# Performance work log

Hardware: AMD Instinct MI355X
Metric: run time of the kernel (lower is better)

## Reference

```python
import jax, jax.numpy as jnp
import numpy as np

BS, S, D, N, E = 16, 8, 10, 32, 300
H, STATE_DIM, MID, OC = 128, 96, 256, 100

def setup_inputs():
    ks = jax.random.split(jax.random.key(0), 24)
    g = lambda i, shape: (0.02 * jax.random.normal(ks[i], shape)).astype(jnp.float32)
    return {
        "stock_news": jax.random.normal(ks[0], (BS, S, D, N, E), dtype=jnp.float32),
        "stock_feats": jax.random.normal(ks[1], (BS, STATE_DIM), dtype=jnp.float32),
        "conv_w3": g(2, (S, OC, E, 3)), "conv_b3": g(3, (S, OC)),
        "conv_w4": g(4, (S, OC, E, 4)), "conv_b4": g(5, (S, OC)),
        "conv_w5": g(6, (S, OC, E, 5)), "conv_b5": g(7, (S, OC)),
        "w_ih": g(8, (S, 4 * H, 3 * OC)), "w_hh": g(9, (S, 4 * H, H)),
        "b_ih": g(10, (S, 4 * H)), "b_hh": g(11, (S, 4 * H)),
        "linX_w": g(12, (S, H, 2 * H)), "linX_b": g(13, (S, H)),
        "linY_w": g(14, (S, 64, H)), "linY_b": g(15, (S, 64)),
        "w1": g(16, (24, STATE_DIM)), "b1": g(17, (24,)),
        "w2": g(18, (16, 24)), "b2": g(19, (16,)),
        "arch_w1": g(20, (MID, 16 + 64 * S)), "arch_b1": g(21, (MID,)),
        "arch_w2": g(22, (S, MID)), "arch_b2": g(23, (S,)),
        "action_var": jnp.full((S,), -0.25, dtype=jnp.float32),
    }

def _conv_maxpool(x, w, b, k):
    # x: [S,B,D,N,E], w: [S,OC,E,k] -> conv1d over news axis then max-pool -> [S,B,D,OC]
    L = x.shape[3] - k + 1
    y = jnp.broadcast_to(b[:, None, None, None, :], (x.shape[0], x.shape[1], x.shape[2], L, w.shape[1]))
    for j in range(k):
        y = y + jnp.einsum('sbdne,soe->sbdno', x[:, :, :, j:j + L, :], w[:, :, :, j])
    return y.max(axis=3)

def _lstm_attn(xs, w_ih, w_hh, b_ih, b_hh):
    # single-stock LSTM (batch_first) + attention from original code; xs: [B,D,I] -> [B,2H]
    pre = jnp.einsum('bdi,gi->dbg', xs, w_ih) + b_ih + b_hh  # [D,B,4H]
    h0 = jnp.zeros((xs.shape[0], w_hh.shape[1]), xs.dtype)
    def step(carry, g_t):
        h, c = carry
        gates = g_t + h @ w_hh.T
        i, f, g, o = jnp.split(gates, 4, axis=-1)  # PyTorch gate order i,f,g,o
        c = jax.nn.sigmoid(f) * c + jax.nn.sigmoid(i) * jnp.tanh(g)
        h = jax.nn.sigmoid(o) * jnp.tanh(c)
        return (h, c), h
    (hn, _), outs = jax.lax.scan(step, (h0, h0), pre)
    outs = outs.transpose(1, 0, 2)  # [B,D,H]
    w = jnp.einsum('bh,bdh->bd', hn, outs)[:, None, :]  # [B,1,D]
    w = jax.nn.softmax(w, axis=1)  # softmax over singleton dim, exactly as torch code (yields ones)
    out = jnp.sum(w.transpose(0, 2, 1) * outs, axis=1)  # [B,H]
    return jnp.concatenate([hn, out], axis=-1)  # [B,2H]

def _forward(stock_news, stock_feats, conv_w3, conv_b3, conv_w4, conv_b4, conv_w5, conv_b5,
             w_ih, w_hh, b_ih, b_hh, linX_w, linX_b, linY_w, linY_b,
             w1, b1, w2, b2, arch_w1, arch_b1, arch_w2, arch_b2, action_var):
    x = stock_news.transpose(1, 0, 2, 3, 4)  # [S,B,D,N,E]
    feats = [_conv_maxpool(x, w, b, k) for (w, b, k) in
             ((conv_w3, conv_b3, 3), (conv_w4, conv_b4, 4), (conv_w5, conv_b5, 5))]
    text = jnp.concatenate(feats, axis=-1)  # [S,B,D,300]
    comb = jax.vmap(_lstm_attn)(text, w_ih, w_hh, b_ih, b_hh)  # [S,B,2H]
    hX = jax.nn.relu(jnp.einsum('sbi,shi->sbh', comb, linX_w) + linX_b[:, None, :])  # dropout is eval-mode identity
    hY = jax.nn.relu(jnp.einsum('sbh,soh->sbo', hX, linY_w) + linY_b[:, None, :])  # [S,B,64]
    stock_text = hY.transpose(1, 0, 2).reshape(stock_news.shape[0], -1)  # [B,S*64]
    f = jax.nn.relu(stock_feats @ w1.T + b1) @ w2.T + b2  # [B,16]
    total = jnp.concatenate([stock_text, f], axis=-1)  # [B,16+64S]
    mu = jnp.tanh(jax.nn.relu(total @ arch_w1.T + arch_b1) @ arch_w2.T + arch_b2)
    return mu, jnp.exp(action_var)

def reference(stock_news, stock_feats, conv_w3, conv_b3, conv_w4, conv_b4, conv_w5, conv_b5,
              w_ih, w_hh, b_ih, b_hh, linX_w, linX_b, linY_w, linY_b,
              w1, b1, w2, b2, arch_w1, arch_b1, arch_w2, arch_b2, action_var):
    return _forward(stock_news, stock_feats, conv_w3, conv_b3, conv_w4, conv_b4, conv_w5, conv_b5,
                    w_ih, w_hh, b_ih, b_hh, linX_w, linX_b, linY_w, linY_b,
                    w1, b1, w2, b2, arch_w1, arch_b1, arch_w2, arch_b2, action_var)
```

## Files before the change

kernel.cpp:

```cpp
#include <hip/hip_runtime.h>
#include <math.h>

#define S_   8
#define B_   16
#define D_   10
#define N_   32
#define E_   300
#define H_   128
#define G4_  512
#define SDIM_ 96
#define MID_ 256
#define TOT_ 528

#define NWPACK 3850240
#define NWPRE  1310720

typedef unsigned short u16;
typedef __attribute__((ext_vector_type(8))) short short8;
typedef __attribute__((ext_vector_type(4))) short short4v;
typedef __attribute__((ext_vector_type(4))) float f32x4;

static __device__ __forceinline__ u16 f2bf(float f) {
    unsigned u = __builtin_bit_cast(unsigned, f);
    return (u16)((u + 0x7FFFu + ((u >> 16) & 1u)) >> 16);
}

__global__ void prep(const float* __restrict__ w3, const float* __restrict__ b3,
                     const float* __restrict__ w4, const float* __restrict__ b4,
                     const float* __restrict__ w5, const float* __restrict__ b5,
                     const float* __restrict__ w_ih,
                     const float* __restrict__ lxw, const float* __restrict__ lyw,
                     const float* __restrict__ aw1,
                     u16* __restrict__ wpack2, u16* __restrict__ wpre2,
                     float* __restrict__ bcomb,
                     float* __restrict__ lxwT, float* __restrict__ lywT,
                     float* __restrict__ aw1T) {
    int idx = blockIdx.x * blockDim.x + threadIdx.x;
    if (idx < NWPACK) {
        int j = idx & 7, q = (idx >> 3) & 3;
        int rest = idx >> 5;
        int c = rest % 320, ks = (rest / 320) % 47, s = rest / 15040;
        int kk = ks * 32 + q * 8 + j;
        int tap = kk / 300, e = kk - tap * 300;
        float v = 0.f;
        if (tap < 5) {
            if (c < 100)      { if (tap < 3) v = w3[((s*100 + c      )*300 + e)*3 + tap]; }
            else if (c < 200) { if (tap < 4) v = w4[((s*100 + c - 100)*300 + e)*4 + tap]; }
            else if (c < 300) {              v = w5[((s*100 + c - 200)*300 + e)*5 + tap]; }
        }
        wpack2[idx] = f2bf(v);
    } else if (idx < NWPACK + NWPRE) {
        int i2 = idx - NWPACK;
        int j = i2 & 7, q = (i2 >> 3) & 3;
        int rest = i2 >> 5;
        int g = rest & 511, ks = (rest >> 9) % 10, s = rest / 5120;
        int kk = ks * 32 + q * 8 + j;
        float v = (kk < 300) ? w_ih[((size_t)s * 512 + g) * 300 + kk] : 0.f;
        wpre2[i2] = f2bf(v);
    }
    if (idx < 262144) {
        int t = idx & 127, i = (idx >> 7) & 255, s = idx >> 15;
        lxwT[idx] = lxw[((size_t)(s * 128 + t)) * 256 + i];
    }
    if (idx < 65536) {
        int t = idx & 63, i = (idx >> 6) & 127, s = idx >> 13;
        lywT[idx] = lyw[((size_t)(s * 64 + t)) * 128 + i];
    }
    if (idx < 135168) {
        int j = idx & 255, i = idx >> 8;
        aw1T[idx] = aw1[(size_t)j * TOT_ + i];
    }
    if (idx < 2560) {
        int c = idx % 320, s = idx / 320;
        float bv = 0.f;
        if (c < 100)      bv = b3[s*100 + c];
        else if (c < 200) bv = b4[s*100 + c - 100];
        else if (c < 300) bv = b5[s*100 + c - 200];
        bcomb[idx] = bv;
    }
}

__global__ __launch_bounds__(256, 2) void conv_mfma(const float* __restrict__ news,
                                                    const u16* __restrict__ wpack2,
                                                    const float* __restrict__ bcomb,
                                                    u16* __restrict__ text_bf) {
    __shared__ u16 xs[2 * 10816];
    const int tid = threadIdx.x, bid = blockIdx.x;
    const int s = bid & 7, b2d = bid >> 3, b2 = b2d / 10, d = b2d % 10;
    const int l = tid & 63, w = tid >> 6, q = l >> 4, r16 = l & 15;

    const u16* gp[5];
#pragma unroll
    for (int nt = 0; nt < 5; ++nt) {
        int c = w * 80 + nt * 16 + r16;
        gp[nt] = wpack2 + (size_t)s * 481280 + c * 32 + q * 8;
    }

    short8 bf0[5], bf1[5];
#pragma unroll
    for (int nt = 0; nt < 5; ++nt) bf0[nt] = *reinterpret_cast<const short8*>(gp[nt]);
#pragma unroll
    for (int nt = 0; nt < 5; ++nt) bf1[nt] = *reinterpret_cast<const short8*>(gp[nt] + 10240);

#pragma unroll
    for (int sm = 0; sm < 2; ++sm) {
        const float4* xg = reinterpret_cast<const float4*>(
            news + (size_t)(((b2 * 2 + sm) * 8 + s) * 10 + d) * 9600);
        for (int i = tid; i < 2704; i += 256) {
            ushort4 u;
            if (i < 2400) {
                float4 v = xg[i];
                u.x = f2bf(v.x); u.y = f2bf(v.y); u.z = f2bf(v.z); u.w = f2bf(v.w);
            } else { u.x = 0; u.y = 0; u.z = 0; u.w = 0; }
            *reinterpret_cast<ushort4*>(&xs[sm * 10816 + 4 * i]) = u;
        }
    }
    __syncthreads();

    f32x4 acc[4][5];
#pragma unroll
    for (int m = 0; m < 4; ++m)
#pragma unroll
        for (int nt = 0; nt < 5; ++nt) acc[m][nt] = (f32x4)(0.f);

#define LOADA(dst, ks) do {                                                     \
    _Pragma("unroll")                                                           \
    for (int m_ = 0; m_ < 4; ++m_) {                                            \
        int off_ = (m_ >> 1) * 10816 + ((m_ & 1) * 16 + r16) * 300 + (ks) * 32 + q * 8; \
        short4v lo_ = *reinterpret_cast<const short4v*>(&xs[off_]);             \
        short4v hi_ = *reinterpret_cast<const short4v*>(&xs[off_ + 4]);         \
        dst[m_] = __builtin_shufflevector(lo_, hi_, 0, 1, 2, 3, 4, 5, 6, 7);    \
    } } while (0)

#define MFMAS(bfv, av) do {                                                     \
    __builtin_amdgcn_s_setprio(1);                                              \
    _Pragma("unroll")                                                           \
    for (int m_ = 0; m_ < 4; ++m_)                                              \
        _Pragma("unroll")                                                       \
        for (int nt_ = 0; nt_ < 5; ++nt_)                                       \
            acc[m_][nt_] = __builtin_amdgcn_mfma_f32_16x16x32_bf16(av[m_], bfv[nt_], acc[m_][nt_], 0, 0, 0); \
    __builtin_amdgcn_s_setprio(0);                                              \
    } while (0)

    short8 a0[4], a1[4];
    LOADA(a0, 0);
    for (int ks = 0; ks < 46; ks += 2) {
        LOADA(a1, ks + 1);
        MFMAS(bf0, a0);
#pragma unroll
        for (int nt = 0; nt < 5; ++nt)
            bf0[nt] = *reinterpret_cast<const short8*>(gp[nt] + (ks + 2) * 10240);

        LOADA(a0, ks + 2);
        MFMAS(bf1, a1);
        if (ks + 3 < 47) {
#pragma unroll
            for (int nt = 0; nt < 5; ++nt)
                bf1[nt] = *reinterpret_cast<const short8*>(gp[nt] + (ks + 3) * 10240);
        }
    }
    MFMAS(bf0, a0);
#undef LOADA
#undef MFMAS

#pragma unroll
    for (int sm = 0; sm < 2; ++sm) {
        const size_t trow = ((size_t)(s * 16 + b2 * 2 + sm) * 10 + d) * 320;
#pragma unroll
        for (int nt = 0; nt < 5; ++nt) {
            int oc = w * 80 + nt * 16 + r16;
            int L = (oc < 100) ? 30 : (oc < 200) ? 29 : 28;
            float mx = -3e38f;
#pragma unroll
            for (int r = 0; r < 4; ++r) {
                mx = fmaxf(mx, acc[sm * 2][nt][r]);
                int row1 = 16 + q * 4 + r;
                if (row1 < L) mx = fmaxf(mx, acc[sm * 2 + 1][nt][r]);
            }
            mx = fmaxf(mx, __shfl_xor(mx, 16));
            mx = fmaxf(mx, __shfl_xor(mx, 32));
            if (l < 16)
                text_bf[trow + oc] = f2bf(mx + bcomb[s * 320 + oc]);
        }
    }
}

__global__ __launch_bounds__(256) void lstm_pre_mfma(const u16* __restrict__ text_bf,
                                                     const u16* __restrict__ wpre2,
                                                     const float* __restrict__ b_ih,
                                                     const float* __restrict__ b_hh,
                                                     float* __restrict__ pre) {
    __shared__ u16 as16[16 * 320];
    const int sd = blockIdx.x, s = sd / 10, d = sd % 10;
    const int tid = threadIdx.x, l = tid & 63, w = tid >> 6, q = l >> 4, r16 = l & 15;

    for (int i = tid; i < 640; i += 256) {
        int r = i / 40, c = i % 40;
        *reinterpret_cast<float4*>(as16 + r * 320 + ((c ^ (r & 7)) << 3)) =
            *reinterpret_cast<const float4*>(text_bf + ((size_t)(s * 16 + r) * 10 + d) * 320 + c * 8);
    }
    __syncthreads();

    const u16* gpb[8];
#pragma unroll
    for (int nt = 0; nt < 8; ++nt) {
        int g = w * 128 + nt * 16 + r16;
        gpb[nt] = wpre2 + (size_t)s * 163840 + g * 32 + q * 8;
    }

    f32x4 acc[8];
#pragma unroll
    for (int nt = 0; nt < 8; ++nt) acc[nt] = (f32x4)(0.f);

    for (int ks = 0; ks < 10; ++ks) {
        short8 a = *reinterpret_cast<const short8*>(
            as16 + r16 * 320 + (((ks * 4 + q) ^ (r16 & 7)) << 3));
#pragma unroll
        for (int nt = 0; nt < 8; ++nt) {
            short8 bf = *reinterpret_cast<const short8*>(gpb[nt] + ks * 16384);
            acc[nt] = __builtin_amdgcn_mfma_f32_16x16x32_bf16(a, bf, acc[nt], 0, 0, 0);
        }
    }

#pragma unroll
    for (int nt = 0; nt < 8; ++nt) {
        int g = w * 128 + nt * 16 + r16;
        float bias = b_ih[s * 512 + g] + b_hh[s * 512 + g];
#pragma unroll
        for (int r = 0; r < 4; ++r) {
            int brow = q * 4 + r;
            pre[((size_t)sd * 16 + brow) * 512 + g] = acc[nt][r] + bias;
        }
    }
}

__global__ __launch_bounds__(512) void lstm_tail(const float* __restrict__ pre,
                                                 const float* __restrict__ w_hh,
                                                 const float* __restrict__ lxwT, const float* __restrict__ lxb,
                                                 const float* __restrict__ lywT, const float* __restrict__ lyb,
                                                 float* __restrict__ total) {
    __shared__ float wchunk[128][129];
    __shared__ float h_lds[H_];
    __shared__ float gates[G4_];
    __shared__ float comb_l[256];
    __shared__ __align__(16) float hx[H_];
    const int sb = blockIdx.x;
    const int s = sb / B_, b = sb % B_;
    const int t = threadIdx.x;

    float wrs[128];
    for (int c = 0; c < 4; ++c) {
        for (int i2 = t; i2 < 128 * 32; i2 += 512) {
            int row = i2 >> 5, fq = i2 & 31;
            float4 v = *reinterpret_cast<const float4*>(
                w_hh + ((size_t)(s * G4_ + c * 128 + row)) * H_ + fq * 4);
            wchunk[row][fq * 4 + 0] = v.x; wchunk[row][fq * 4 + 1] = v.y;
            wchunk[row][fq * 4 + 2] = v.z; wchunk[row][fq * 4 + 3] = v.w;
        }
        __syncthreads();
        if ((t >> 7) == c) {
            int r = t & 127;
#pragma unroll
            for (int i = 0; i < 128; ++i) wrs[i] = wchunk[r][i];
        }
        __syncthreads();
    }

    float cc = 0.f, hsum = 0.f, hval = 0.f;
    if (t < H_) h_lds[t] = 0.f;
    __syncthreads();

    for (int d = 0; d < D_; ++d) {
        float a0 = pre[(((size_t)(s * D_ + d) * B_ + b)) * G4_ + t];
        float a1 = 0.f, a2 = 0.f, a3 = 0.f;
#pragma unroll
        for (int i = 0; i < 128; i += 4) {
            float4 h4 = *reinterpret_cast<const float4*>(&h_lds[i]);
            a0 = fmaf(wrs[i + 0], h4.x, a0);
            a1 = fmaf(wrs[i + 1], h4.y, a1);
            a2 = fmaf(wrs[i + 2], h4.z, a2);
            a3 = fmaf(wrs[i + 3], h4.w, a3);
        }
        gates[t] = (a0 + a1) + (a2 + a3);
        __syncthreads();
        if (t < H_) {
            float ig = 1.f / (1.f + expf(-gates[t]));
            float fg = 1.f / (1.f + expf(-gates[H_ + t]));
            float gg = tanhf(gates[2 * H_ + t]);
            float og = 1.f / (1.f + expf(-gates[3 * H_ + t]));
            cc = fg * cc + ig * gg;
            hval = og * tanhf(cc);
            hsum += hval;
            h_lds[t] = hval;
        }
        __syncthreads();
    }
    if (t < H_) { comb_l[t] = hval; comb_l[H_ + t] = hsum; }
    __syncthreads();
    if (t < H_) {
        const float* wv = lxwT + (size_t)s * 256 * 128 + t;
        float a0 = lxb[s * H_ + t], a1 = 0.f;
        for (int i = 0; i < 256; i += 2) {
            a0 = fmaf(comb_l[i], wv[(size_t)i * 128], a0);
            a1 = fmaf(comb_l[i + 1], wv[(size_t)(i + 1) * 128], a1);
        }
        hx[t] = fmaxf(a0 + a1, 0.f);
    }
    __syncthreads();
    if (t < 64) {
        const float* wv = lywT + (size_t)s * 128 * 64 + t;
        float a0 = lyb[s * 64 + t], a1 = 0.f;
        for (int i = 0; i < 128; i += 2) {
            a0 = fmaf(hx[i], wv[(size_t)i * 64], a0);
            a1 = fmaf(hx[i + 1], wv[(size_t)(i + 1) * 64], a1);
        }
        total[(size_t)b * 512 + s * 64 + t] = fmaxf(a0 + a1, 0.f);
    }
}

__global__ __launch_bounds__(256) void head_feats(const float* __restrict__ total,
                                                  const float* __restrict__ sf,
                                                  const float* __restrict__ w1, const float* __restrict__ b1,
                                                  const float* __restrict__ w2, const float* __restrict__ b2,
                                                  const float* __restrict__ aw1T, const float* __restrict__ ab1,
                                                  const float* __restrict__ aw2, const float* __restrict__ ab2,
                                                  const float* __restrict__ avar,
                                                  float* __restrict__ out) {
    __shared__ __align__(16) float tr[TOT_];
    __shared__ float hid[MID_];
    __shared__ float h1f[24];
    const int bb = blockIdx.x, t = threadIdx.x;
    if (t < 128)
        reinterpret_cast<float4*>(tr)[t] = reinterpret_cast<const float4*>(total + (size_t)bb * 512)[t];
    if (t < 24) {
        float acc = b1[t];
        for (int i = 0; i < SDIM_; ++i) acc = fmaf(sf[bb * SDIM_ + i], w1[t * SDIM_ + i], acc);
        h1f[t] = fmaxf(acc, 0.f);
    }
    __syncthreads();
    if (t < 16) {
        float acc = b2[t];
        for (int i = 0; i < 24; ++i) acc = fmaf(h1f[i], w2[t * 24 + i], acc);
        tr[512 + t] = acc;
    }
    __syncthreads();
    {
        const float* wv = aw1T + t;
        float a0 = ab1[t], a1 = 0.f, a2 = 0.f, a3 = 0.f;
        for (int i = 0; i < TOT_; i += 4) {
            a0 = fmaf(tr[i + 0], wv[(size_t)(i + 0) * 256], a0);
            a1 = fmaf(tr[i + 1], wv[(size_t)(i + 1) * 256], a1);
            a2 = fmaf(tr[i + 2], wv[(size_t)(i + 2) * 256], a2);
            a3 = fmaf(tr[i + 3], wv[(size_t)(i + 3) * 256], a3);
        }
        hid[t] = fmaxf((a0 + a1) + (a2 + a3), 0.f);
    }
    __syncthreads();
    if (t < 8) {
        float acc = ab2[t];
        const float* wv = aw2 + (size_t)t * MID_;
        for (int i = 0; i < MID_; ++i) acc = fmaf(hid[i], wv[i], acc);
        out[bb * 8 + t] = tanhf(acc);
    }
    if (bb == 0 && t >= 8 && t < 16) out[128 + (t - 8)] = expf(avar[t - 8]);
}

extern "C" void kernel_launch(void* const* d_in, const int* in_sizes, int n_in,
                              void* d_out, int out_size, void* d_ws, size_t ws_size,
                              hipStream_t stream) {
    const float* news = (const float*)d_in[0];
    const float* sf   = (const float*)d_in[1];
    const float* w3   = (const float*)d_in[2];  const float* b3 = (const float*)d_in[3];
    const float* w4   = (const float*)d_in[4];  const float* b4 = (const float*)d_in[5];
    const float* w5   = (const float*)d_in[6];  const float* b5 = (const float*)d_in[7];
    const float* w_ih = (const float*)d_in[8];  const float* w_hh = (const float*)d_in[9];
    const float* b_ih = (const float*)d_in[10]; const float* b_hh = (const float*)d_in[11];
    const float* lxw  = (const float*)d_in[12]; const float* lxb = (const float*)d_in[13];
    const float* lyw  = (const float*)d_in[14]; const float* lyb = (const float*)d_in[15];
    const float* w1   = (const float*)d_in[16]; const float* b1 = (const float*)d_in[17];
    const float* w2   = (const float*)d_in[18]; const float* b2 = (const float*)d_in[19];
    const float* aw1  = (const float*)d_in[20]; const float* ab1 = (const float*)d_in[21];
    const float* aw2  = (const float*)d_in[22]; const float* ab2 = (const float*)d_in[23];
    const float* avar = (const float*)d_in[24];

    char* ws = (char*)d_ws;
    u16*   wpack2  = (u16*)ws;
    u16*   wpre2   = (u16*)(ws + 7700480);
    float* bcomb   = (float*)(ws + 10321920);
    u16*   text_bf = (u16*)(ws + 10332160);
    float* pre     = (float*)(ws + 11151360);
    float* total   = (float*)(ws + 13772800);
    float* lxwT    = (float*)(ws + 13805568);
    float* lywT    = (float*)(ws + 14854144);
    float* aw1T    = (float*)(ws + 15116288);

    prep<<<(NWPACK + NWPRE + 255) / 256, 256, 0, stream>>>(w3, b3, w4, b4, w5, b5, w_ih,
                                                           lxw, lyw, aw1,
                                                           wpack2, wpre2, bcomb, lxwT, lywT, aw1T);
    conv_mfma<<<640, 256, 0, stream>>>(news, wpack2, bcomb, text_bf);
    lstm_pre_mfma<<<S_ * D_, 256, 0, stream>>>(text_bf, wpre2, b_ih, b_hh, pre);
    lstm_tail<<<S_ * B_, 512, 0, stream>>>(pre, w_hh, lxwT, lxb, lywT, lyb, total);
    head_feats<<<B_, 256, 0, stream>>>(total, sf, w1, b1, w2, b2, aw1T, ab1, aw2, ab2, avar, (float*)d_out);
}
```

Before: 134.4 us.

## Retile conv kernel to 512-thread blocks covering five days with more weight reuse

The conv MFMA kernel now uses 256 blocks of 8 waves, each holding five days of one batch/stock in LDS. Each wave covers five M-tiles against five N-tiles, so every B-fragment load from global memory feeds more MFMAs. Row-half maxima are combined through a shared partial buffer before the bf16 store. The head kernel also splits the 528-long dot product across two thread halves. The cost is higher LDS use (about 108KB plus partials), which may reduce occupancy, and only 256 blocks to spread across the CUs.

```diff
diff --git a/kernel.cpp b/kernel.cpp
--- a/kernel.cpp
+++ b/kernel.cpp
@@ -80,19 +80,22 @@
     }
 }
 
-__global__ __launch_bounds__(256, 2) void conv_mfma(const float* __restrict__ news,
+__global__ __launch_bounds__(512, 2) void conv_mfma(const float* __restrict__ news,
                                                     const u16* __restrict__ wpack2,
                                                     const float* __restrict__ bcomb,
                                                     u16* __restrict__ text_bf) {
-    __shared__ u16 xs[2 * 10816];
+    __shared__ u16 xs[5 * 10816];
+    __shared__ float part[10][320];
     const int tid = threadIdx.x, bid = blockIdx.x;
-    const int s = bid & 7, b2d = bid >> 3, b2 = b2d / 10, d = b2d % 10;
-    const int l = tid & 63, w = tid >> 6, q = l >> 4, r16 = l & 15;
+    const int s = bid & 7, rr_ = bid >> 3, b = rr_ >> 1, half = rr_ & 1;
+    const int l = tid & 63, wvi = tid >> 6;
+    const int wm = wvi >> 2, wn = wvi & 3;
+    const int q = l >> 4, r16 = l & 15;
 
     const u16* gp[5];
 #pragma unroll
     for (int nt = 0; nt < 5; ++nt) {
-        int c = w * 80 + nt * 16 + r16;
+        int c = wn * 80 + nt * 16 + r16;
         gp[nt] = wpack2 + (size_t)s * 481280 + c * 32 + q * 8;
     }
 
@@ -102,56 +105,56 @@
 #pragma unroll
     for (int nt = 0; nt < 5; ++nt) bf1[nt] = *reinterpret_cast<const short8*>(gp[nt] + 10240);
 
-#pragma unroll
-    for (int sm = 0; sm < 2; ++sm) {
+    for (int day = 0; day < 5; ++day) {
         const float4* xg = reinterpret_cast<const float4*>(
-            news + (size_t)(((b2 * 2 + sm) * 8 + s) * 10 + d) * 9600);
-        for (int i = tid; i < 2704; i += 256) {
+            news + (size_t)((b * 8 + s) * 10 + half * 5 + day) * 9600);
+        for (int i = tid; i < 2704; i += 512) {
             ushort4 u;
             if (i < 2400) {
                 float4 v = xg[i];
                 u.x = f2bf(v.x); u.y = f2bf(v.y); u.z = f2bf(v.z); u.w = f2bf(v.w);
             } else { u.x = 0; u.y = 0; u.z = 0; u.w = 0; }
-            *reinterpret_cast<ushort4*>(&xs[sm * 10816 + 4 * i]) = u;
-        }
-    }
-    __syncthreads();
-
-    f32x4 acc[4][5];
-#pragma unroll
-    for (int m = 0; m < 4; ++m)
-#pragma unroll
-        for (int nt = 0; nt < 5; ++nt) acc[m][nt] = (f32x4)(0.f);
-
-#define LOADA(dst, ks) do {                                                     \
-    _Pragma("unroll")                                                           \
-    for (int m_ = 0; m_ < 4; ++m_) {                                            \
-        int off_ = (m_ >> 1) * 10816 + ((m_ & 1) * 16 + r16) * 300 + (ks) * 32 + q * 8; \
-        short4v lo_ = *reinterpret_cast<const short4v*>(&xs[off_]);             \
-        short4v hi_ = *reinterpret_cast<const short4v*>(&xs[off_ + 4]);         \
-        dst[m_] = __builtin_shufflevector(lo_, hi_, 0, 1, 2, 3, 4, 5, 6, 7);    \
+            *reinterpret_cast<ushort4*>(&xs[day * 10816 + 4 * i]) = u;
+        }
+    }
+    __syncthreads();
+
+    f32x4 acc[5][5];
+#pragma unroll
+    for (int mt = 0; mt < 5; ++mt)
+#pragma unroll
+        for (int nt = 0; nt < 5; ++nt) acc[mt][nt] = (f32x4)(0.f);
+
+#define LOADA(dst, ks) do {                                                       \
+    _Pragma("unroll")                                                             \
+    for (int mt_ = 0; mt_ < 5; ++mt_) {                                           \
+        int di_ = wm * 5 + mt_;                                                   \
+        int off_ = (di_ >> 1) * 10816 + (((di_ & 1) << 4) + r16) * 300            \
+                   + (ks) * 32 + q * 8;                                           \
+        short4v lo_ = *reinterpret_cast<const short4v*>(&xs[off_]);               \
+        short4v hi_ = *reinterpret_cast<const short4v*>(&xs[off_ + 4]);           \
+        dst[mt_] = __builtin_shufflevector(lo_, hi_, 0, 1, 2, 3, 4, 5, 6, 7);     \
     } } while (0)
 
-#define MFMAS(bfv, av) do {                                                     \
-    __builtin_amdgcn_s_setprio(1);                                              \
-    _Pragma("unroll")                                                           \
-    for (int m_ = 0; m_ < 4; ++m_)                                              \
-        _Pragma("unroll")                                                       \
-        for (int nt_ = 0; nt_ < 5; ++nt_)                                       \
-            acc[m_][nt_] = __builtin_amdgcn_mfma_f32_16x16x32_bf16(av[m_], bfv[nt_], acc[m_][nt_], 0, 0, 0); \
-    __builtin_amdgcn_s_setprio(0);                                              \
+#define MFMAS(bfv, av) do {                                                       \
+    __builtin_amdgcn_s_setprio(1);                                                \
+    _Pragma("unroll")                                                             \
+    for (int nt_ = 0; nt_ < 5; ++nt_)                                             \
+        _Pragma("unroll")                                                         \
+        for (int mt_ = 0; mt_ < 5; ++mt_)                                         \
+            acc[mt_][nt_] = __builtin_amdgcn_mfma_f32_16x16x32_bf16(av[mt_], bfv[nt_], acc[mt_][nt_], 0, 0, 0); \
+    __builtin_amdgcn_s_setprio(0);                                                \
     } while (0)
 
-    short8 a0[4], a1[4];
-    LOADA(a0, 0);
     for (int ks = 0; ks < 46; ks += 2) {
-        LOADA(a1, ks + 1);
+        short8 a0[5], a1[5];
+        LOADA(a0, ks);
         MFMAS(bf0, a0);
 #pragma unroll
         for (int nt = 0; nt < 5; ++nt)
             bf0[nt] = *reinterpret_cast<const short8*>(gp[nt] + (ks + 2) * 10240);
 
-        LOADA(a0, ks + 2);
+        LOADA(a1, ks + 1);
         MFMAS(bf1, a1);
         if (ks + 3 < 47) {
 #pragma unroll
@@ -159,29 +162,39 @@
                 bf1[nt] = *reinterpret_cast<const short8*>(gp[nt] + (ks + 3) * 10240);
         }
     }
-    MFMAS(bf0, a0);
+    {
+        short8 a0[5];
+        LOADA(a0, 46);
+        MFMAS(bf0, a0);
+    }
 #undef LOADA
 #undef MFMAS
 
 #pragma unroll
-    for (int sm = 0; sm < 2; ++sm) {
-        const size_t trow = ((size_t)(s * 16 + b2 * 2 + sm) * 10 + d) * 320;
+    for (int mt = 0; mt < 5; ++mt) {
+        const int di = wm * 5 + mt;
+        const int nwb = (di & 1) << 4;
 #pragma unroll
         for (int nt = 0; nt < 5; ++nt) {
-            int oc = w * 80 + nt * 16 + r16;
+            int oc = wn * 80 + nt * 16 + r16;
             int L = (oc < 100) ? 30 : (oc < 200) ? 29 : 28;
             float mx = -3e38f;
 #pragma unroll
-            for (int r = 0; r < 4; ++r) {
-                mx = fmaxf(mx, acc[sm * 2][nt][r]);
-                int row1 = 16 + q * 4 + r;
-                if (row1 < L) mx = fmaxf(mx, acc[sm * 2 + 1][nt][r]);
+            for (int rr = 0; rr < 4; ++rr) {
+                int nw = nwb + q * 4 + rr;
+                if (nw < L) mx = fmaxf(mx, acc[mt][nt][rr]);
             }
             mx = fmaxf(mx, __shfl_xor(mx, 16));
             mx = fmaxf(mx, __shfl_xor(mx, 32));
-            if (l < 16)
-                text_bf[trow + oc] = f2bf(mx + bcomb[s * 320 + oc]);
-        }
+            if (l < 16) part[di][wn * 80 + nt * 16 + l] = mx;
+        }
+    }
+    __syncthreads();
+    for (int i = tid; i < 1600; i += 512) {
+        int day = i / 320, oc = i - day * 320;
+        float mx = fmaxf(part[2 * day][oc], part[2 * day + 1][oc]);
+        text_bf[((size_t)(s * 16 + b) * 10 + half * 5 + day) * 320 + oc] =
+            f2bf(mx + bcomb[s * 320 + oc]);
     }
 }
 
@@ -318,7 +331,7 @@
     }
 }
 
-__global__ __launch_bounds__(256) void head_feats(const float* __restrict__ total,
+__global__ __launch_bounds__(512) void head_feats(const float* __restrict__ total,
                                                   const float* __restrict__ sf,
                                                   const float* __restrict__ w1, const float* __restrict__ b1,
                                                   const float* __restrict__ w2, const float* __restrict__ b2,
@@ -329,6 +342,7 @@
     __shared__ __align__(16) float tr[TOT_];
     __shared__ float hid[MID_];
     __shared__ float h1f[24];
+    __shared__ float pA[MID_], pB[MID_];
     const int bb = blockIdx.x, t = threadIdx.x;
     if (t < 128)
         reinterpret_cast<float4*>(tr)[t] = reinterpret_cast<const float4*>(total + (size_t)bb * 512)[t];
@@ -345,16 +359,21 @@
     }
     __syncthreads();
     {
-        const float* wv = aw1T + t;
-        float a0 = ab1[t], a1 = 0.f, a2 = 0.f, a3 = 0.f;
-        for (int i = 0; i < TOT_; i += 4) {
+        const int j = t & 255, hf = t >> 8;
+        const int ilo = hf ? 264 : 0, ihi = hf ? 528 : 264;
+        const float* wv = aw1T + j;
+        float a0 = 0.f, a1 = 0.f, a2 = 0.f, a3 = 0.f;
+        for (int i = ilo; i < ihi; i += 4) {
             a0 = fmaf(tr[i + 0], wv[(size_t)(i + 0) * 256], a0);
             a1 = fmaf(tr[i + 1], wv[(size_t)(i + 1) * 256], a1);
             a2 = fmaf(tr[i + 2], wv[(size_t)(i + 2) * 256], a2);
             a3 = fmaf(tr[i + 3], wv[(size_t)(i + 3) * 256], a3);
         }
-        hid[t] = fmaxf((a0 + a1) + (a2 + a3), 0.f);
-    }
+        float p = (a0 + a1) + (a2 + a3);
+        if (hf) pB[j] = p; else pA[j] = p;
+    }
+    __syncthreads();
+    if (t < MID_) hid[t] = fmaxf(pA[t] + pB[t] + ab1[t], 0.f);
     __syncthreads();
     if (t < 8) {
         float acc = ab2[t];
@@ -397,8 +416,8 @@
     prep<<<(NWPACK + NWPRE + 255) / 256, 256, 0, stream>>>(w3, b3, w4, b4, w5, b5, w_ih,
                                                            lxw, lyw, aw1,
                                                            wpack2, wpre2, bcomb, lxwT, lywT, aw1T);
-    conv_mfma<<<640, 256, 0, stream>>>(news, wpack2, bcomb, text_bf);
+    conv_mfma<<<256, 512, 0, stream>>>(news, wpack2, bcomb, text_bf);
     lstm_pre_mfma<<<S_ * D_, 256, 0, stream>>>(text_bf, wpre2, b_ih, b_hh, pre);
     lstm_tail<<<S_ * B_, 512, 0, stream>>>(pre, w_hh, lxwT, lxb, lywT, lyb, total);
-    head_feats<<<B_, 256, 0, stream>>>(total, sf, w1, b1, w2, b2, aw1T, ab1, aw2, ab2, avar, (float*)d_out);
-}
+    head_feats<<<B_, 512, 0, stream>>>(total, sf, w1, b1, w2, b2, aw1T, ab1, aw2, ab2, avar, (float*)d_out);
+}
```

Result: no change. 135.8 us (+1.0%).
